# Kernel tuning notes

Measured on AMD Instinct MI355X. Metric: run time of the kernel, lower is better.

## Reference

```python
import jax, jax.numpy as jnp
import numpy as np

N = 524288   # predicate-expression nodes
M = N // 2   # binary-formula nodes
L = 50       # self.length
VOCAB = 100  # max_embeddings
OUT = 3 * L + 5  # output_size = 155


def _attention(x, W_att, b_att):
    # x: [B, k, L]. torch Attention: softmax over the stacked-args axis, weighted sum.
    logits = jnp.einsum('bkl,lo->bko', x, W_att) + b_att   # [B, k, 1]
    a = jax.nn.softmax(logits, axis=1)
    return jnp.sum(a * x, axis=1)                           # [B, L]


def setup_inputs() -> dict:
    key = jax.random.key(0)
    ks = jax.random.split(key, 20)
    s = 0.05
    inp = {
        'pe': jax.random.normal(ks[0], (VOCAB, L), jnp.float32),
        've': jax.random.normal(ks[1], (VOCAB, L), jnp.float32),
        'oe': jax.random.normal(ks[2], (VOCAB, L), jnp.float32),
        'W_pred': jax.random.normal(ks[3], (6 * L, L), jnp.float32) * s,
        'b_pred': jax.random.normal(ks[4], (L,), jnp.float32) * s,
        'W_bin': jax.random.normal(ks[5], (3 * L, L), jnp.float32) * s,
        'b_bin': jax.random.normal(ks[6], (L,), jnp.float32) * s,
        'W_un': jax.random.normal(ks[7], (L, L), jnp.float32) * s,
        'b_un': jax.random.normal(ks[8], (L,), jnp.float32) * s,
        'W_univ': jax.random.normal(ks[9], (L, L), jnp.float32) * s,
        'b_univ': jax.random.normal(ks[10], (L,), jnp.float32) * s,
        'W_att': jax.random.normal(ks[11], (L, 1), jnp.float32) * s,
        'b_att': jax.random.normal(ks[12], (1,), jnp.float32) * s,
        'W_fin': jax.random.normal(ks[13], (L, OUT), jnp.float32) * s,
        'b_fin': jax.random.normal(ks[14], (OUT,), jnp.float32) * s,
        'pred_ids': jax.random.randint(ks[15], (N,), 0, VOCAB),
        'var_ids': jax.random.randint(ks[16], (N, 5), 0, VOCAB),
        'op_ids': jax.random.randint(ks[17], (M,), 0, VOCAB),
    }
    return inp


def reference(pe, ve, oe, W_pred, b_pred, W_bin, b_bin, W_un, b_un,
              W_univ, b_univ, W_att, b_att, W_fin, b_fin,
              pred_ids, var_ids, op_ids):
    # visit_predicate_expression, batched: [predicate_emb, 5 arg embs] -> [N, 6, L]
    args = jnp.concatenate([pe[pred_ids][:, None, :], ve[var_ids]], axis=1)
    h_pred = (jax.nn.relu(args.reshape(N, 6 * L) @ W_pred + b_pred)
              + _attention(args, W_att, b_att))                      # [N, L]

    # visit_binary_formula, batched over adjacent pairs: [left, op, right]
    ops = jnp.stack([h_pred[0::2], oe[op_ids], h_pred[1::2]], axis=1)  # [M, 3, L]
    h_bin = (jax.nn.relu(ops.reshape(M, 3 * L) @ W_bin + b_bin)
             + _attention(ops, W_att, b_att))                         # [M, L]

    # visit_unary_formula, then universal quantified formula
    h_un = jax.nn.relu(h_bin @ W_un + b_un)
    h_q = jax.nn.relu(h_un @ W_univ + b_univ)

    # final projection: forward() -> self.final(...)
    return h_q @ W_fin + b_fin  # [M, OUT]
```

## Files before the change

kernel.cpp:

```cpp
#include <hip/hip_runtime.h>
#include <hip/hip_fp16.h>

#define LDIM 50
#define MBIN 262144
#define ODIM 155
#define VOCABSZ 100

typedef _Float16 f16x4 __attribute__((ext_vector_type(4)));
typedef _Float16 f16x2 __attribute__((ext_vector_type(2)));
typedef float    f32x4 __attribute__((ext_vector_type(4)));

static __device__ __forceinline__ __half2 relu2(__half2 a) {
    f16x2 av; __builtin_memcpy(&av, &a, sizeof(av));
    const f16x2 zv = {(_Float16)0.0f, (_Float16)0.0f};
    f16x2 r = __builtin_elementwise_max(av, zv);
    __half2 out; __builtin_memcpy(&out, &r, sizeof(out));
    return out;
}

#define H_TBL  0
#define H_TO   44800
#define H_WC   54800
#define H_WU   62224
#define H_WV   66576
#define H_WF   70928
#define F_LG   40960

#define LB_SLAB 0
#define LB_WC   29696
#define LB_WU   44544
#define LB_WV   53248
#define LB_OP   61952
#define LB_W0   64000
#define LB_W2   66048
#define LB_W1   68096
#define LB_BU   70144
#define LB_BV   70400
#define LB_BF   70656
#define LB_LG   71296
#define LB_WATT 72512
#define LDS_BYTES 72640

__global__ __launch_bounds__(256) void precompute_kernel(
    const float* __restrict__ pe, const float* __restrict__ ve, const float* __restrict__ oe,
    const float* __restrict__ W_pred, const float* __restrict__ b_pred,
    const float* __restrict__ W_bin, const float* __restrict__ b_bin,
    const float* __restrict__ W_un, const float* __restrict__ W_univ,
    const float* __restrict__ W_fin,
    const float* __restrict__ W_att, const float* __restrict__ b_att,
    float* __restrict__ ws)
{
    __half* wsh = (__half*)ws;
    const int bid = blockIdx.x, tid = threadIdx.x;
    if (bid < 150) {
        const int row = bid*4 + (tid >> 6);
        const int t = tid & 63;
        const int s = row / VOCABSZ, v = row % VOCABSZ;
        if (t < 56) {
            float acc = 0.0f;
            if (t < 50) {
                acc = (s == 0) ? b_pred[t] : 0.0f;
                const float* E = (s == 0) ? pe : ve;
#pragma unroll
                for (int e = 0; e < 50; ++e)
                    acc += E[v*50 + e] * W_pred[(s*50 + e)*50 + t];
            }
            wsh[H_TBL + row*56 + t] = __float2half_rn(acc);
        }
    } else if (bid < 152) {
        const int which = bid - 150;
        const float* E = which ? ve : pe;
        const int base = H_TBL + (600 + which*100) * 56;
        for (int idx = tid; idx < 5600; idx += 256) {
            const int r = idx / 56, c = idx % 56;
            wsh[base + idx] = __float2half_rn((c < 50) ? E[r*50 + c] : 0.0f);
        }
    } else if (bid < 177) {
        const int v = (bid - 152)*4 + (tid >> 6);
        const int t = tid & 63;
        if (t < 50) {
            float acc = b_bin[t];
#pragma unroll
            for (int e = 0; e < 50; ++e)
                acc += oe[v*50 + e] * W_bin[(50 + e)*50 + t];
            wsh[H_TO + (v*50 + t)*2]     = __float2half_rn(acc);
            wsh[H_TO + (v*50 + t)*2 + 1] = __float2half_rn(oe[v*50 + t]);
        }
    } else if (bid == 177) {
        const int n = tid & 63, kc = tid >> 6;
        for (int k = kc*29; k < kc*29 + 29; ++k) {
            float val = 0.0f;
            if (n < 50) {
                if (k < 50)       val = W_bin[k*50 + n];
                else if (k < 100) val = W_bin[(100 + k - 50)*50 + n];
            }
            wsh[H_WC + n*116 + k] = __float2half_rn(val);
        }
    } else if (bid == 178) {
        const int n = tid & 63;
        const int half = tid >> 7;
        const int kc = (tid >> 6) & 1;
        const float* W = half ? W_univ : W_un;
        const int base = half ? H_WV : H_WU;
        for (int k = kc*34; k < kc*34 + 34; ++k) {
            float val = (n < 50 && k < 50) ? W[k*50 + n] : 0.0f;
            wsh[base + n*68 + k] = __float2half_rn(val);
        }
    } else if (bid == 179) {
        for (int idx = tid; idx < 10880; idx += 256) {
            const int n = idx % 160, k = idx / 160;
            float val = (n < ODIM && k < 50) ? W_fin[k*ODIM + n] : 0.0f;
            wsh[H_WF + n*68 + k] = __float2half_rn(val);
        }
    } else {
        for (int g = tid; g < 300; g += 256) {
            const int which = g / VOCABSZ, v = g % VOCABSZ;
            const float* E = (which == 0) ? pe : ((which == 1) ? ve : oe);
            float acc = b_att[0];
#pragma unroll
            for (int e = 0; e < 50; ++e)
                acc += E[v*50 + e] * W_att[e];
            ws[F_LG + g] = acc;
        }
    }
}

__device__ __forceinline__ float build_node(
    int p, const int* __restrict__ v, __half2 e02, const __half2* __restrict__ ek2,
    __half2 invs, const uint4* __restrict__ tq, const __half2* __restrict__ wattl,
    __half2* __restrict__ h2out)
{
    const __half2 z2 = __floats2half2_rn(0.0f, 0.0f);
    __half2 lacc = z2;
#pragma unroll
    for (int g = 0; g < 7; ++g) {
        uint4 ul = tq[p*7 + g];
        uint4 up = tq[(600 + p)*7 + g];
        __half2 lin[4], num[4];
#pragma unroll
        for (int k = 0; k < 4; ++k) {
            lin[k] = ((const __half2*)&ul)[k];
            num[k] = __hmul2(e02, ((const __half2*)&up)[k]);
        }
#pragma unroll
        for (int s = 0; s < 5; ++s) {
            uint4 ua = tq[((s+1)*VOCABSZ + v[s])*7 + g];
            uint4 uv = tq[(700 + v[s])*7 + g];
#pragma unroll
            for (int k = 0; k < 4; ++k) {
                lin[k] = __hadd2(lin[k], ((const __half2*)&ua)[k]);
                num[k] = __hfma2(ek2[s], ((const __half2*)&uv)[k], num[k]);
            }
        }
#pragma unroll
        for (int k = 0; k < 4; ++k) {
            const __half2 h = __hfma2(num[k], invs, relu2(lin[k]));
            h2out[g*4 + k] = h;
            lacc = __hfma2(h, wattl[g*4 + k], lacc);
        }
    }
    return __low2float(lacc) + __high2float(lacc);
}

__global__ __launch_bounds__(512)
void fused_kernel(
    const float* __restrict__ W_att, const float* __restrict__ b_att,
    const float* __restrict__ b_un, const float* __restrict__ b_univ,
    const float* __restrict__ b_fin,
    const int* __restrict__ pred_ids, const int* __restrict__ var_ids,
    const int* __restrict__ op_ids,
    const float* __restrict__ ws, float* __restrict__ out)
{
    __shared__ __align__(16) char ldsraw[LDS_BYTES];
    const __half* wsh = (const __half*)ws;
    const int tid = threadIdx.x;
    const int w = tid >> 6, l = tid & 63;
    const int lr = l & 15, q = l >> 4;
    const int jbase = blockIdx.x * 512;

    int*   opl = (int*)(ldsraw + LB_OP);
    float* w0l = (float*)(ldsraw + LB_W0);
    float* w2l = (float*)(ldsraw + LB_W2);
    float* w1l = (float*)(ldsraw + LB_W1);
    float* bul = (float*)(ldsraw + LB_BU);
    float* bvl = (float*)(ldsraw + LB_BV);
    float* bfl = (float*)(ldsraw + LB_BF);
    float* lgl = (float*)(ldsraw + LB_LG);

    {
        const uint4* sc = (const uint4*)(wsh + H_WC);
        uint4* dc = (uint4*)(ldsraw + LB_WC);
        for (int i = tid; i < 928; i += 512) dc[i] = sc[i];
        const uint4* su = (const uint4*)(wsh + H_WU);
        uint4* du = (uint4*)(ldsraw + LB_WU);
        for (int i = tid; i < 544; i += 512) du[i] = su[i];
        const uint4* sv = (const uint4*)(wsh + H_WV);
        uint4* dv = (uint4*)(ldsraw + LB_WV);
        for (int i = tid; i < 544; i += 512) dv[i] = sv[i];
        if (tid < 300) lgl[tid] = ws[F_LG + tid];
        if (tid < LDIM) { bul[tid] = b_un[tid]; bvl[tid] = b_univ[tid]; }
        if (tid < ODIM) bfl[tid] = b_fin[tid];
        if (tid >= 256 && tid < 284) {
            const int i = tid - 256;
            const float x = (2*i < 50)   ? W_att[2*i]   : 0.0f;
            const float y = (2*i+1 < 50) ? W_att[2*i+1] : 0.0f;
            ((__half2*)(ldsraw + LB_WATT))[i] = __floats2half2_rn(x, y);
        }
    }
    __syncthreads();

    const int j = jbase + tid;
    int vA[5], vB[5];
    const int pA = pred_ids[2*j], pB = pred_ids[2*j+1];
#pragma unroll
    for (int s = 0; s < 5; ++s) { vA[s] = var_ids[(2*j)*5 + s]; vB[s] = var_ids[(2*j+1)*5 + s]; }
    const int op = op_ids[j];

    float ekA[5], ekB[5];
    const float e0A = __expf(lgl[pA]);
    const float e0B = __expf(lgl[pB]);
    float denA = e0A, denB = e0B;
#pragma unroll
    for (int s = 0; s < 5; ++s) {
        ekA[s] = __expf(lgl[VOCABSZ + vA[s]]); denA += ekA[s];
        ekB[s] = __expf(lgl[VOCABSZ + vB[s]]); denB += ekB[s];
    }
    const float invA = 1.0f / denA, invB = 1.0f / denB;
    const float batt = b_att[0];

    __half2 ek2A[5], ek2B[5];
#pragma unroll
    for (int s = 0; s < 5; ++s) {
        ek2A[s] = __float2half2_rn(ekA[s]);
        ek2B[s] = __float2half2_rn(ekB[s]);
    }

    const uint4* tq = (const uint4*)wsh;
    const __half2* wattl = (const __half2*)(ldsraw + LB_WATT);

    __half2 hA2[28], hB2[28];
    const float w0 = __expf(batt + build_node(pA, vA, __float2half2_rn(e0A), ek2A,
                                              __float2half2_rn(invA), tq, wattl, hA2));
    const float w2 = __expf(batt + build_node(pB, vB, __float2half2_rn(e0B), ek2B,
                                              __float2half2_rn(invB), tq, wattl, hB2));
    const float w1 = __expf(lgl[2*VOCABSZ + op]);
    const float inv2 = 1.0f / (w0 + w1 + w2);

    opl[tid] = op;
    w0l[tid] = w0*inv2; w2l[tid] = w2*inv2; w1l[tid] = w1*inv2;

    char* slab = ldsraw + LB_SLAB + w*3712;
    const __half2* TOg = (const __half2*)(wsh + H_TO);
    const _Float16* Wcp = (const _Float16*)(ldsraw + LB_WC);
    const _Float16* Wup = (const _Float16*)(ldsraw + LB_WU);
    const _Float16* Wvp = (const _Float16*)(ldsraw + LB_WV);
    const _Float16* Wfg = (const _Float16*)(wsh + H_WF);

    for (int c = 0; c < 4; ++c) {
        if ((l >> 4) == c) {
            uint* dst = (uint*)(slab + (l & 15)*232);
#pragma unroll
            for (int i = 0; i < 25; ++i) { uint u; __builtin_memcpy(&u, &hA2[i], 4); dst[i] = u; }
#pragma unroll
            for (int i = 0; i < 25; ++i) { uint u; __builtin_memcpy(&u, &hB2[i], 4); dst[25+i] = u; }
#pragma unroll
            for (int i = 50; i < 58; ++i) dst[i] = 0u;
        }

        f32x4 C1[4];
#pragma unroll
        for (int nt = 0; nt < 4; ++nt) C1[nt] = (f32x4){0.f, 0.f, 0.f, 0.f};
#pragma unroll
        for (int kk = 0; kk < 7; ++kk) {
            f16x4 a = *(const f16x4*)(slab + lr*232 + kk*32 + q*8);
#pragma unroll
            for (int nt = 0; nt < 4; ++nt) {
                f16x4 b = *(const f16x4*)((const char*)Wcp + (nt*16 + lr)*232 + kk*32 + q*8);
                C1[nt] = __builtin_amdgcn_mfma_f32_16x16x16f16(a, b, C1[nt], 0, 0, 0);
            }
        }
        {
            const __half* sh = (const __half*)slab;
            const int cb = c*16;
#pragma unroll
            for (int nt = 0; nt < 4; ++nt) {
                const int d = nt*16 + lr;
#pragma unroll
                for (int r = 0; r < 4; ++r) {
                    float v = 0.0f;
                    if (d < LDIM) {
                        const int nw = w*64 + cb + q*4 + r;
                        const int opn = opl[nw];
                        const float2 to = __half22float2(TOg[opn*LDIM + d]);
                        const float hAv = __half2float(sh[(q*4 + r)*116 + d]);
                        const float hBv = __half2float(sh[(q*4 + r)*116 + 50 + d]);
                        v = fmaxf(C1[nt][r] + to.x, 0.0f)
                          + w0l[nw]*hAv + w2l[nw]*hBv + w1l[nw]*to.y;
                    }
                    C1[nt][r] = v;
                }
            }
            __half* shw = (__half*)slab;
#pragma unroll
            for (int nt = 0; nt < 4; ++nt)
#pragma unroll
                for (int r = 0; r < 4; ++r)
                    shw[(q*4 + r)*116 + nt*16 + lr] = __float2half(C1[nt][r]);
        }

        {
            f32x4 C2[4];
#pragma unroll
            for (int nt = 0; nt < 4; ++nt) C2[nt] = (f32x4){0.f, 0.f, 0.f, 0.f};
#pragma unroll
            for (int kk = 0; kk < 4; ++kk) {
                f16x4 a = *(const f16x4*)(slab + lr*232 + kk*32 + q*8);
#pragma unroll
                for (int nt = 0; nt < 4; ++nt) {
                    f16x4 b = *(const f16x4*)((const char*)Wup + (nt*16 + lr)*136 + kk*32 + q*8);
                    C2[nt] = __builtin_amdgcn_mfma_f32_16x16x16f16(a, b, C2[nt], 0, 0, 0);
                }
            }
            __half* shw = (__half*)slab;
#pragma unroll
            for (int nt = 0; nt < 4; ++nt) {
                const int d = nt*16 + lr;
#pragma unroll
                for (int r = 0; r < 4; ++r) {
                    const float v = (d < LDIM) ? fmaxf(C2[nt][r] + bul[d], 0.0f) : 0.0f;
                    shw[(q*4 + r)*116 + d] = __float2half(v);
                }
            }
        }

        {
            f32x4 C3[4];
#pragma unroll
            for (int nt = 0; nt < 4; ++nt) C3[nt] = (f32x4){0.f, 0.f, 0.f, 0.f};
#pragma unroll
            for (int kk = 0; kk < 4; ++kk) {
                f16x4 a = *(const f16x4*)(slab + lr*232 + kk*32 + q*8);
#pragma unroll
                for (int nt = 0; nt < 4; ++nt) {
                    f16x4 b = *(const f16x4*)((const char*)Wvp + (nt*16 + lr)*136 + kk*32 + q*8);
                    C3[nt] = __builtin_amdgcn_mfma_f32_16x16x16f16(a, b, C3[nt], 0, 0, 0);
                }
            }
            __half* shw = (__half*)slab;
#pragma unroll
            for (int nt = 0; nt < 4; ++nt) {
                const int d = nt*16 + lr;
#pragma unroll
                for (int r = 0; r < 4; ++r) {
                    const float v = (d < LDIM) ? fmaxf(C3[nt][r] + bvl[d], 0.0f) : 0.0f;
                    shw[(q*4 + r)*116 + d] = __float2half(v);
                }
            }
        }

        {
            float* gb = out + (size_t)(jbase + w*64 + c*16) * ODIM;
            for (int nt = 0; nt < 10; ++nt) {
                f16x4 bf[4];
#pragma unroll
                for (int kk = 0; kk < 4; ++kk)
                    bf[kk] = *(const f16x4*)((const char*)Wfg + (nt*16 + lr)*136 + kk*32 + q*8);
                f32x4 c4 = (f32x4){0.f, 0.f, 0.f, 0.f};
#pragma unroll
                for (int kk = 0; kk < 4; ++kk) {
                    f16x4 a = *(const f16x4*)(slab + lr*232 + kk*32 + q*8);
                    c4 = __builtin_amdgcn_mfma_f32_16x16x16f16(a, bf[kk], c4, 0, 0, 0);
                }
                const int o = nt*16 + lr;
                const float bv = (o < ODIM) ? bfl[o] : 0.0f;
#pragma unroll
                for (int r = 0; r < 4; ++r)
                    *(float*)(slab + (q*4 + r)*232 + 128 + lr*4) = c4[r] + bv;
#pragma unroll
                for (int it = 0; it < 4; ++it) {
                    const int row = it*4 + q;
                    if (o < ODIM)
                        gb[row*ODIM + nt*16 + lr] =
                            *(const float*)(slab + row*232 + 128 + lr*4);
                }
            }
        }
    }
}

extern "C" void kernel_launch(void* const* d_in, const int* in_sizes, int n_in,
                              void* d_out, int out_size, void* d_ws, size_t ws_size,
                              hipStream_t stream) {
    const float* pe     = (const float*)d_in[0];
    const float* ve     = (const float*)d_in[1];
    const float* oe     = (const float*)d_in[2];
    const float* W_pred = (const float*)d_in[3];
    const float* b_pred = (const float*)d_in[4];
    const float* W_bin  = (const float*)d_in[5];
    const float* b_bin  = (const float*)d_in[6];
    const float* W_un   = (const float*)d_in[7];
    const float* b_un   = (const float*)d_in[8];
    const float* W_univ = (const float*)d_in[9];
    const float* b_univ = (const float*)d_in[10];
    const float* W_att  = (const float*)d_in[11];
    const float* b_att  = (const float*)d_in[12];
    const float* W_fin  = (const float*)d_in[13];
    const float* b_fin  = (const float*)d_in[14];
    const int* pred_ids = (const int*)d_in[15];
    const int* var_ids  = (const int*)d_in[16];
    const int* op_ids   = (const int*)d_in[17];
    float* out = (float*)d_out;
    float* ws  = (float*)d_ws;

    precompute_kernel<<<181, 256, 0, stream>>>(pe, ve, oe, W_pred, b_pred,
                                               W_bin, b_bin, W_un, W_univ, W_fin,
                                               W_att, b_att, ws);
    fused_kernel<<<MBIN/512, 512, 0, stream>>>(W_att, b_att, b_un, b_univ, b_fin,
                                               pred_ids, var_ids, op_ids, ws, out);
}
```

Before: 311.4 us.

## Drop LDS weight staging, shrink blocks to 128 threads with per-wave LDS

Stops copying the bin/unary/universal weight matrices, biases and attention logits into shared memory and reads them straight from the global workspace, relying on the cache. LDS per block drops to two small per-wave slabs and blocks shrink from 512 to 128 threads with no block-wide barrier. The aim is to remove the per-block staging prologue and sync and to raise occupancy. The cost is that MFMA B-operand loads now come from global/L2 instead of LDS, which may add latency.

```diff
diff --git a/kernel.cpp b/kernel.cpp
--- a/kernel.cpp
+++ b/kernel.cpp
@@ -24,22 +24,11 @@
 #define H_WU   62224
 #define H_WV   66576
 #define H_WF   70928
+#define H_WATT 81808
 #define F_LG   40960
 
-#define LB_SLAB 0
-#define LB_WC   29696
-#define LB_WU   44544
-#define LB_WV   53248
-#define LB_OP   61952
-#define LB_W0   64000
-#define LB_W2   66048
-#define LB_W1   68096
-#define LB_BU   70144
-#define LB_BV   70400
-#define LB_BF   70656
-#define LB_LG   71296
-#define LB_WATT 72512
-#define LDS_BYTES 72640
+#define LB_WAVE 4736
+#define LDS_BYTES (2*LB_WAVE)
 
 __global__ __launch_bounds__(256) void precompute_kernel(
     const float* __restrict__ pe, const float* __restrict__ ve, const float* __restrict__ oe,
@@ -122,6 +111,11 @@
                 acc += E[v*50 + e] * W_att[e];
             ws[F_LG + g] = acc;
         }
+        if (tid < 28) {
+            const float x = (2*tid < 50)   ? W_att[2*tid]   : 0.0f;
+            const float y = (2*tid+1 < 50) ? W_att[2*tid+1] : 0.0f;
+            ((__half2*)(wsh + H_WATT))[tid] = __floats2half2_rn(x, y);
+        }
     }
 }
 
@@ -162,9 +156,9 @@
     return __low2float(lacc) + __high2float(lacc);
 }
 
-__global__ __launch_bounds__(512)
+__global__ __launch_bounds__(128, 4)
 void fused_kernel(
-    const float* __restrict__ W_att, const float* __restrict__ b_att,
+    const float* __restrict__ b_att,
     const float* __restrict__ b_un, const float* __restrict__ b_univ,
     const float* __restrict__ b_fin,
     const int* __restrict__ pred_ids, const int* __restrict__ var_ids,
@@ -176,40 +170,19 @@
     const int tid = threadIdx.x;
     const int w = tid >> 6, l = tid & 63;
     const int lr = l & 15, q = l >> 4;
-    const int jbase = blockIdx.x * 512;
-
-    int*   opl = (int*)(ldsraw + LB_OP);
-    float* w0l = (float*)(ldsraw + LB_W0);
-    float* w2l = (float*)(ldsraw + LB_W2);
-    float* w1l = (float*)(ldsraw + LB_W1);
-    float* bul = (float*)(ldsraw + LB_BU);
-    float* bvl = (float*)(ldsraw + LB_BV);
-    float* bfl = (float*)(ldsraw + LB_BF);
-    float* lgl = (float*)(ldsraw + LB_LG);
-
-    {
-        const uint4* sc = (const uint4*)(wsh + H_WC);
-        uint4* dc = (uint4*)(ldsraw + LB_WC);
-        for (int i = tid; i < 928; i += 512) dc[i] = sc[i];
-        const uint4* su = (const uint4*)(wsh + H_WU);
-        uint4* du = (uint4*)(ldsraw + LB_WU);
-        for (int i = tid; i < 544; i += 512) du[i] = su[i];
-        const uint4* sv = (const uint4*)(wsh + H_WV);
-        uint4* dv = (uint4*)(ldsraw + LB_WV);
-        for (int i = tid; i < 544; i += 512) dv[i] = sv[i];
-        if (tid < 300) lgl[tid] = ws[F_LG + tid];
-        if (tid < LDIM) { bul[tid] = b_un[tid]; bvl[tid] = b_univ[tid]; }
-        if (tid < ODIM) bfl[tid] = b_fin[tid];
-        if (tid >= 256 && tid < 284) {
-            const int i = tid - 256;
-            const float x = (2*i < 50)   ? W_att[2*i]   : 0.0f;
-            const float y = (2*i+1 < 50) ? W_att[2*i+1] : 0.0f;
-            ((__half2*)(ldsraw + LB_WATT))[i] = __floats2half2_rn(x, y);
-        }
-    }
-    __syncthreads();
-
-    const int j = jbase + tid;
+    const int jwb = blockIdx.x*128 + w*64;
+    const int j = jwb + l;
+
+    char* wbase = ldsraw + w*LB_WAVE;
+    char* slab  = wbase;
+    int*   opw = (int*)(wbase + 3712);
+    float* w0w = (float*)(wbase + 3968);
+    float* w2w = (float*)(wbase + 4224);
+    float* w1w = (float*)(wbase + 4480);
+
+    const float* lgf = ws + F_LG;
+    const float batt = b_att[0];
+
     int vA[5], vB[5];
     const int pA = pred_ids[2*j], pB = pred_ids[2*j+1];
 #pragma unroll
@@ -217,16 +190,15 @@
     const int op = op_ids[j];
 
     float ekA[5], ekB[5];
-    const float e0A = __expf(lgl[pA]);
-    const float e0B = __expf(lgl[pB]);
+    const float e0A = __expf(lgf[pA]);
+    const float e0B = __expf(lgf[pB]);
     float denA = e0A, denB = e0B;
 #pragma unroll
     for (int s = 0; s < 5; ++s) {
-        ekA[s] = __expf(lgl[VOCABSZ + vA[s]]); denA += ekA[s];
-        ekB[s] = __expf(lgl[VOCABSZ + vB[s]]); denB += ekB[s];
+        ekA[s] = __expf(lgf[VOCABSZ + vA[s]]); denA += ekA[s];
+        ekB[s] = __expf(lgf[VOCABSZ + vB[s]]); denB += ekB[s];
     }
     const float invA = 1.0f / denA, invB = 1.0f / denB;
-    const float batt = b_att[0];
 
     __half2 ek2A[5], ek2B[5];
 #pragma unroll
@@ -236,25 +208,24 @@
     }
 
     const uint4* tq = (const uint4*)wsh;
-    const __half2* wattl = (const __half2*)(ldsraw + LB_WATT);
+    const __half2* wattg = (const __half2*)(wsh + H_WATT);
 
     __half2 hA2[28], hB2[28];
     const float w0 = __expf(batt + build_node(pA, vA, __float2half2_rn(e0A), ek2A,
-                                              __float2half2_rn(invA), tq, wattl, hA2));
+                                              __float2half2_rn(invA), tq, wattg, hA2));
     const float w2 = __expf(batt + build_node(pB, vB, __float2half2_rn(e0B), ek2B,
-                                              __float2half2_rn(invB), tq, wattl, hB2));
-    const float w1 = __expf(lgl[2*VOCABSZ + op]);
+                                              __float2half2_rn(invB), tq, wattg, hB2));
+    const float w1 = __expf(lgf[2*VOCABSZ + op]);
     const float inv2 = 1.0f / (w0 + w1 + w2);
 
-    opl[tid] = op;
-    w0l[tid] = w0*inv2; w2l[tid] = w2*inv2; w1l[tid] = w1*inv2;
-
-    char* slab = ldsraw + LB_SLAB + w*3712;
+    opw[l] = op;
+    w0w[l] = w0*inv2; w2w[l] = w2*inv2; w1w[l] = w1*inv2;
+
     const __half2* TOg = (const __half2*)(wsh + H_TO);
-    const _Float16* Wcp = (const _Float16*)(ldsraw + LB_WC);
-    const _Float16* Wup = (const _Float16*)(ldsraw + LB_WU);
-    const _Float16* Wvp = (const _Float16*)(ldsraw + LB_WV);
-    const _Float16* Wfg = (const _Float16*)(wsh + H_WF);
+    const char* Wcg = (const char*)(wsh + H_WC);
+    const char* Wug = (const char*)(wsh + H_WU);
+    const char* Wvg = (const char*)(wsh + H_WV);
+    const char* Wfg = (const char*)(wsh + H_WF);
 
     for (int c = 0; c < 4; ++c) {
         if ((l >> 4) == c) {
@@ -275,7 +246,7 @@
             f16x4 a = *(const f16x4*)(slab + lr*232 + kk*32 + q*8);
 #pragma unroll
             for (int nt = 0; nt < 4; ++nt) {
-                f16x4 b = *(const f16x4*)((const char*)Wcp + (nt*16 + lr)*232 + kk*32 + q*8);
+                f16x4 b = *(const f16x4*)(Wcg + (nt*16 + lr)*232 + kk*32 + q*8);
                 C1[nt] = __builtin_amdgcn_mfma_f32_16x16x16f16(a, b, C1[nt], 0, 0, 0);
             }
         }
@@ -289,13 +260,13 @@
                 for (int r = 0; r < 4; ++r) {
                     float v = 0.0f;
                     if (d < LDIM) {
-                        const int nw = w*64 + cb + q*4 + r;
-                        const int opn = opl[nw];
+                        const int nw = cb + q*4 + r;
+                        const int opn = opw[nw];
                         const float2 to = __half22float2(TOg[opn*LDIM + d]);
                         const float hAv = __half2float(sh[(q*4 + r)*116 + d]);
                         const float hBv = __half2float(sh[(q*4 + r)*116 + 50 + d]);
                         v = fmaxf(C1[nt][r] + to.x, 0.0f)
-                          + w0l[nw]*hAv + w2l[nw]*hBv + w1l[nw]*to.y;
+                          + w0w[nw]*hAv + w2w[nw]*hBv + w1w[nw]*to.y;
                     }
                     C1[nt][r] = v;
                 }
@@ -317,7 +288,7 @@
                 f16x4 a = *(const f16x4*)(slab + lr*232 + kk*32 + q*8);
 #pragma unroll
                 for (int nt = 0; nt < 4; ++nt) {
-                    f16x4 b = *(const f16x4*)((const char*)Wup + (nt*16 + lr)*136 + kk*32 + q*8);
+                    f16x4 b = *(const f16x4*)(Wug + (nt*16 + lr)*136 + kk*32 + q*8);
                     C2[nt] = __builtin_amdgcn_mfma_f32_16x16x16f16(a, b, C2[nt], 0, 0, 0);
                 }
             }
@@ -325,9 +296,10 @@
 #pragma unroll
             for (int nt = 0; nt < 4; ++nt) {
                 const int d = nt*16 + lr;
+                const float bu = (d < LDIM) ? b_un[d] : 0.0f;
 #pragma unroll
                 for (int r = 0; r < 4; ++r) {
-                    const float v = (d < LDIM) ? fmaxf(C2[nt][r] + bul[d], 0.0f) : 0.0f;
+                    const float v = (d < LDIM) ? fmaxf(C2[nt][r] + bu, 0.0f) : 0.0f;
                     shw[(q*4 + r)*116 + d] = __float2half(v);
                 }
             }
@@ -342,7 +314,7 @@
                 f16x4 a = *(const f16x4*)(slab + lr*232 + kk*32 + q*8);
 #pragma unroll
                 for (int nt = 0; nt < 4; ++nt) {
-                    f16x4 b = *(const f16x4*)((const char*)Wvp + (nt*16 + lr)*136 + kk*32 + q*8);
+                    f16x4 b = *(const f16x4*)(Wvg + (nt*16 + lr)*136 + kk*32 + q*8);
                     C3[nt] = __builtin_amdgcn_mfma_f32_16x16x16f16(a, b, C3[nt], 0, 0, 0);
                 }
             }
@@ -350,21 +322,22 @@
 #pragma unroll
             for (int nt = 0; nt < 4; ++nt) {
                 const int d = nt*16 + lr;
+                const float bv = (d < LDIM) ? b_univ[d] : 0.0f;
 #pragma unroll
                 for (int r = 0; r < 4; ++r) {
-                    const float v = (d < LDIM) ? fmaxf(C3[nt][r] + bvl[d], 0.0f) : 0.0f;
+                    const float v = (d < LDIM) ? fmaxf(C3[nt][r] + bv, 0.0f) : 0.0f;
                     shw[(q*4 + r)*116 + d] = __float2half(v);
                 }
             }
         }
 
         {
-            float* gb = out + (size_t)(jbase + w*64 + c*16) * ODIM;
+            float* gb = out + (size_t)(jwb + c*16) * ODIM;
             for (int nt = 0; nt < 10; ++nt) {
                 f16x4 bf[4];
 #pragma unroll
                 for (int kk = 0; kk < 4; ++kk)
-                    bf[kk] = *(const f16x4*)((const char*)Wfg + (nt*16 + lr)*136 + kk*32 + q*8);
+                    bf[kk] = *(const f16x4*)(Wfg + (nt*16 + lr)*136 + kk*32 + q*8);
                 f32x4 c4 = (f32x4){0.f, 0.f, 0.f, 0.f};
 #pragma unroll
                 for (int kk = 0; kk < 4; ++kk) {
@@ -372,7 +345,7 @@
                     c4 = __builtin_amdgcn_mfma_f32_16x16x16f16(a, bf[kk], c4, 0, 0, 0);
                 }
                 const int o = nt*16 + lr;
-                const float bv = (o < ODIM) ? bfl[o] : 0.0f;
+                const float bv = (o < ODIM) ? b_fin[o] : 0.0f;
 #pragma unroll
                 for (int r = 0; r < 4; ++r)
                     *(float*)(slab + (q*4 + r)*232 + 128 + lr*4) = c4[r] + bv;
@@ -415,6 +388,6 @@
     precompute_kernel<<<181, 256, 0, stream>>>(pe, ve, oe, W_pred, b_pred,
                                                W_bin, b_bin, W_un, W_univ, W_fin,
                                                W_att, b_att, ws);
-    fused_kernel<<<MBIN/512, 512, 0, stream>>>(W_att, b_att, b_un, b_univ, b_fin,
+    fused_kernel<<<MBIN/128, 128, 0, stream>>>(b_att, b_un, b_univ, b_fin,
                                                pred_ids, var_ids, op_ids, ws, out);
 }
```

After: 673.0 us. +116.1%, slower.
